# Performance work log

Hardware: AMD Instinct MI355X
Metric: run time of the kernel (lower is better)

The kernel has to match this reference:

```python
import jax, jax.numpy as jnp
import numpy as np

B, C, N = 2, 512, 2048
HEADS, DIM_HEAD, SCALE = 16, 64, 8.0
H_DIM = HEADS * DIM_HEAD
EPS = 1e-12  # F.normalize default eps


def setup_inputs() -> dict:
    key = jax.random.key(0)
    ks = jax.random.split(key, 5)
    x = jax.random.normal(ks[0], (B, C, N), dtype=jnp.float32)
    Wqkv = jax.random.normal(ks[1], (3 * H_DIM, C), dtype=jnp.float32) * (1.0 / np.sqrt(C))
    q_scale = jnp.ones((DIM_HEAD,), dtype=jnp.float32)
    k_scale = jnp.ones((DIM_HEAD,), dtype=jnp.float32)
    Wout = jax.random.normal(ks[2], (C, H_DIM), dtype=jnp.float32) * (1.0 / np.sqrt(H_DIM))
    bout = jax.random.normal(ks[3], (C,), dtype=jnp.float32) * 0.01
    return {"x": x, "Wqkv": Wqkv, "q_scale": q_scale, "k_scale": k_scale,
            "Wout": Wout, "bout": bout}


def _l2norm(t):
    # F.normalize(t, dim=-1): t / max(||t||, eps)
    n = jnp.sqrt(jnp.sum(t * t, axis=-1, keepdims=True))
    return t / jnp.maximum(n, EPS)


def reference(x, Wqkv, q_scale, k_scale, Wout, bout):
    # 1x1 conv == pointwise matmul over channel dim
    qkv = jnp.einsum('oc,bcn->bon', Wqkv, x)              # [B, 3*H_DIM, N]
    q, k, v = jnp.split(qkv, 3, axis=1)
    # unflatten channels -> [B, H, D, N]
    def to_heads(t):
        return t.reshape(B, HEADS, DIM_HEAD, N)
    q, k, v = map(to_heads, (q, k, v))
    # cosine attention: l2-normalize q,k over head dim, apply learned per-dim scales
    q = _l2norm(q.transpose(0, 1, 3, 2)) * q_scale        # [B, H, N, D]
    k = _l2norm(k.transpose(0, 1, 3, 2)) * k_scale        # [B, H, N, D]
    sim = jnp.einsum('bhid,bhjd->bhij', q, k) * SCALE     # [B, H, N, N]
    attn = jax.nn.softmax(sim, axis=-1)
    out = jnp.einsum('bhij,bhdj->bhid', attn, v)          # [B, H, N, D]
    out = out.transpose(0, 1, 3, 2).reshape(B, H_DIM, N)  # b h n d -> b (h d) n
    return jnp.einsum('oc,bcn->bon', Wout, out) + bout[None, :, None]
```

## Files before the change

kernel.cpp:

```cpp
#include <hip/hip_runtime.h>
#include <hip/hip_bf16.h>

#define BATCH 2
#define CCH   512
#define NSEQ  2048
#define HEADS 16
#define DHEAD 64
#define HDIM  1024
#define ODIM  3072
#define QK_PRESCALE 11.541560327111707f

typedef short short4v __attribute__((ext_vector_type(4)));
typedef short short8 __attribute__((ext_vector_type(8)));
typedef float float4v __attribute__((ext_vector_type(4)));
typedef int   int4v   __attribute__((ext_vector_type(4)));

__device__ __forceinline__ unsigned short f2bf(float f) {
    unsigned int u = __float_as_uint(f);
    return (unsigned short)((u + 0x7FFFu + ((u >> 16) & 1u)) >> 16);
}
__device__ __forceinline__ unsigned short f2bf_fast(float f) {
    return (unsigned short)((__float_as_uint(f) + 0x8000u) >> 16);
}
__device__ __forceinline__ float fexp2(float x) {
#if __has_builtin(__builtin_amdgcn_exp2f)
    return __builtin_amdgcn_exp2f(x);
#else
    return exp2f(x);
#endif
}
__device__ __forceinline__ int pack_bf16(float lo, float hi) {
#if __has_builtin(__builtin_amdgcn_cvt_pk_bf16_f32)
    typedef __bf16 bf2_t __attribute__((ext_vector_type(2)));
    bf2_t v = __builtin_amdgcn_cvt_pk_bf16_f32(lo, hi);
    return __builtin_bit_cast(int, v);
#else
    return (int)f2bf_fast(lo) | ((int)(unsigned)f2bf_fast(hi) << 16);
#endif
}

typedef __attribute__((address_space(1))) const void* as1_cvp;
typedef __attribute__((address_space(3))) void* as3_vp;
__device__ __forceinline__ void cp16(const void* g, void* l) {
    __builtin_amdgcn_global_load_lds((as1_cvp)g, (as3_vp)l, 16, 0, 0);
}
__global__ __launch_bounds__(256) void k_prep(
    const float* __restrict__ Wqkv, const float* __restrict__ Wout,
    const float* __restrict__ x,
    const float* __restrict__ qs, const float* __restrict__ ks,
    unsigned short* __restrict__ Wqkvb, unsigned short* __restrict__ Woutb,
    unsigned short* __restrict__ xt, float* __restrict__ M) {
    const int bx = blockIdx.x;
    if (bx < 2048) {
        if (bx == 0 && threadIdx.x < 64) {
            int lane = threadIdx.x;
            float p = fabsf(qs[lane] * ks[lane]);
#pragma unroll
            for (int off = 1; off < 64; off <<= 1) p = fmaxf(p, __shfl_xor(p, off));
            if (lane == 0) *M = QK_PRESCALE * p;
        }
        int i4 = (bx * 256 + threadIdx.x) * 4;
        const float* src; unsigned short* dst; int idx;
        if (i4 < ODIM * CCH) { src = Wqkv; dst = Wqkvb; idx = i4; }
        else { src = Wout; dst = Woutb; idx = i4 - ODIM * CCH; }
        float4 v = *(const float4*)(src + idx);
        ushort4 o;
        o.x = f2bf(v.x); o.y = f2bf(v.y); o.z = f2bf(v.z); o.w = f2bf(v.w);
        *(ushort4*)(dst + idx) = o;
        return;
    }
    __shared__ unsigned short t[64][65];
    const int fx = bx - 2048;
    const int n0 = (fx & 31) * 64;
    const int c0 = ((fx >> 5) & 7) * 64;
    const int b  = fx >> 8;
    const int tr = threadIdx.x >> 6, tc = threadIdx.x & 63;
    const float* xs = x + (size_t)b * CCH * NSEQ;
    unsigned short* xd = xt + (size_t)b * NSEQ * CCH;
#pragma unroll
    for (int r = 0; r < 16; ++r) {
        int c = r * 4 + tr;
        t[c][tc] = f2bf(xs[(size_t)(c0 + c) * NSEQ + n0 + tc]);
    }
    __syncthreads();
#pragma unroll
    for (int r = 0; r < 16; ++r) {
        int n = r * 4 + tr;
        xd[(size_t)(n0 + n) * CCH + c0 + tc] = t[tc][n];
    }
}

__global__ __launch_bounds__(256) void k_gemm_qkv(
    const unsigned short* __restrict__ W, const unsigned short* __restrict__ xt,
    const float* __restrict__ qs, const float* __restrict__ ks,
    unsigned short* __restrict__ qh, unsigned short* __restrict__ kh,
    unsigned short* __restrict__ vb) {
    constexpr int K = CCH, N = NSEQ;
    __shared__ __align__(16) short smem[2 * 128 * 64];
    short* lsA = smem;
    short* lsB = smem + 128 * 64;
    const int tid = threadIdx.x, wave = tid >> 6, lane = tid & 63;
    const int l15 = lane & 15, quad = lane >> 4;
    const int n0 = blockIdx.x * 128, m0 = blockIdx.y * 128, z = blockIdx.z;
    const short* Ab = (const short*)W + (size_t)m0 * K;
    const short* Bb = (const short*)xt + ((size_t)z * N + n0) * K;
    const int wm = wave >> 1, wn = wave & 1;
    const int cswz = (((tid & 7) ^ ((tid >> 3) & 7))) * 8;
    const int sw7 = (l15 & 7);

    float4v acc[4][4];
#pragma unroll
    for (int i = 0; i < 4; ++i)
#pragma unroll
        for (int j = 0; j < 4; ++j) acc[i][j] = (float4v){0.f, 0.f, 0.f, 0.f};

    for (int k0 = 0; k0 < K; k0 += 64) {
#pragma unroll
        for (int it = 0; it < 4; ++it) {
            int row = it * 32 + (tid >> 3);
            cp16(Ab + (size_t)row * K + k0 + cswz, &lsA[it * 2048 + wave * 512]);
            cp16(Bb + (size_t)row * K + k0 + cswz, &lsB[it * 2048 + wave * 512]);
        }
        __syncthreads();
        short8 af[4][2], bfr[4][2];
#pragma unroll
        for (int t = 0; t < 4; ++t)
#pragma unroll
            for (int kk = 0; kk < 2; ++kk) {
                af[t][kk]  = *(const short8*)&lsA[(wm * 64 + t * 16 + l15) * 64 + ((kk * 4 + quad) ^ sw7) * 8];
                bfr[t][kk] = *(const short8*)&lsB[(wn * 64 + t * 16 + l15) * 64 + ((kk * 4 + quad) ^ sw7) * 8];
            }
#pragma unroll
        for (int mt = 0; mt < 4; ++mt)
#pragma unroll
            for (int nt = 0; nt < 4; ++nt) {
                acc[mt][nt] = __builtin_amdgcn_mfma_f32_16x16x32_bf16(af[mt][0], bfr[nt][0], acc[mt][nt], 0, 0, 0);
                acc[mt][nt] = __builtin_amdgcn_mfma_f32_16x16x32_bf16(af[mt][1], bfr[nt][1], acc[mt][nt], 0, 0, 0);
            }
        __syncthreads();
    }

    const int co   = (m0 + wm * 64) >> 6;
    const int part = co >> 4;
    const int h    = co & 15;
    const int bh   = z * HEADS + h;
    short* myT = smem + wave * 4096;

    if (part < 2) {
        float inv[4];
#pragma unroll
        for (int nt = 0; nt < 4; ++nt) {
            float ss = 0.f;
#pragma unroll
            for (int mt = 0; mt < 4; ++mt)
#pragma unroll
                for (int r = 0; r < 4; ++r) ss += acc[mt][nt][r] * acc[mt][nt][r];
            ss += __shfl_xor(ss, 16);
            ss += __shfl_xor(ss, 32);
            inv[nt] = 1.0f / fmaxf(sqrtf(ss), 1e-12f);
        }
        const float* sc = part ? ks : qs;
        const float csc = part ? 1.0f : QK_PRESCALE;
#pragma unroll
        for (int mt = 0; mt < 4; ++mt) {
            const int db = mt * 16 + quad * 4;
            float4 s4 = *(const float4*)(sc + db);
            s4.x *= csc; s4.y *= csc; s4.z *= csc; s4.w *= csc;
#pragma unroll
            for (int nt = 0; nt < 4; ++nt) {
                int nl = nt * 16 + l15;
                short4v o;
                o.x = (short)f2bf(acc[mt][nt][0] * inv[nt] * s4.x);
                o.y = (short)f2bf(acc[mt][nt][1] * inv[nt] * s4.y);
                o.z = (short)f2bf(acc[mt][nt][2] * inv[nt] * s4.z);
                o.w = (short)f2bf(acc[mt][nt][3] * inv[nt] * s4.w);
                *(short4v*)&myT[nl * 64 + (((db >> 3) ^ (nl & 7)) << 3) + (db & 7)] = o;
            }
        }
        unsigned short* dst = (part ? kh : qh) + (size_t)bh * NSEQ * DHEAD
                              + (size_t)(n0 + wn * 64) * DHEAD;
#pragma unroll
        for (int pass = 0; pass < 8; ++pass) {
            int nl = pass * 8 + (lane >> 3), c = lane & 7;
            short8 vv = *(const short8*)&myT[nl * 64 + ((c ^ (nl & 7)) << 3)];
            *(short8*)&dst[(size_t)nl * DHEAD + c * 8] = vv;
        }
    } else {
#pragma unroll
        for (int mt = 0; mt < 4; ++mt)
#pragma unroll
            for (int nt = 0; nt < 4; ++nt) {
                int nl = nt * 16 + l15;
                int swc = nl >> 3, swo = nl & 7;
#pragma unroll
                for (int r = 0; r < 4; ++r) {
                    int d = mt * 16 + quad * 4 + r;
                    myT[d * 64 + ((swc ^ (d & 7)) << 3) + swo] = (short)f2bf(acc[mt][nt][r]);
                }
            }
        unsigned short* dst = vb + (size_t)bh * DHEAD * NSEQ + n0 + wn * 64;
#pragma unroll
        for (int pass = 0; pass < 8; ++pass) {
            int d = pass * 8 + (lane >> 3), c = lane & 7;
            short8 vv = *(const short8*)&myT[d * 64 + ((c ^ (d & 7)) << 3)];
            *(short8*)&dst[(size_t)d * NSEQ + c * 8] = vv;
        }
    }
}

#define KVB 32
__global__ __launch_bounds__(512, 4) void k_attn(
    const unsigned short* __restrict__ qh, const unsigned short* __restrict__ kh,
    const unsigned short* __restrict__ vb,
    unsigned short* __restrict__ aot, const float* __restrict__ Mptr) {
    __shared__ __align__(16) short Kt[2][4][KVB * 64];
    __shared__ __align__(16) short Vt[2][4][64 * KVB];
    const int tid = threadIdx.x, wave = tid >> 6, lane = tid & 63;
    const int grp = wave >> 2, w4 = wave & 3;
    const int gtid = tid & 255;
    const int l15 = lane & 15, quad = lane >> 4, q8 = quad * 8;
    const int flat = blockIdx.x;
    const int xcd = flat & 7, idx = flat >> 3;
    const int bh = xcd * 4 + (idx >> 4);
    const int i0 = (idx & 15) * 128;
    const int b = bh >> 4, h = bh & 15;
    const float Ms = *Mptr;
    const float4v mInit = (float4v){-Ms, -Ms, -Ms, -Ms};
    const int srowK = gtid >> 3;
    const int kkey  = (srowK & 3) | (((srowK >> 3) & 1) << 2);
    const int cswzK = ((gtid & 7) ^ kkey) * 8;
    const int srowV = gtid >> 2;
    const int cswzV = ((gtid & 3) ^ ((srowV >> 1) & 3)) * 8;
    const int ksw = l15 & 7;
    const int kc0 = ((0 + quad) ^ ksw) * 8;
    const int kc1 = ((4 + quad) ^ ksw) * 8;
    const int vkr = (l15 >> 1) & 3;
    const int ar0 = (l15 >> 2) * 8 + (l15 & 3);
    const int ar1 = ar0 + 4;
    const int jbase = grp * (NSEQ / 2);

    short8 qf[2][2];
    {
        const short* qb = (const short*)qh + ((size_t)bh * NSEQ + i0 + w4 * 32) * DHEAD;
#pragma unroll
        for (int it = 0; it < 2; ++it) {
            qf[it][0] = *(const short8*)&qb[(it * 16 + l15) * DHEAD + q8];
            qf[it][1] = *(const short8*)&qb[(it * 16 + l15) * DHEAD + 32 + q8];
        }
    }

    float4v of[2][4];
#pragma unroll
    for (int it = 0; it < 2; ++it)
#pragma unroll
        for (int dt = 0; dt < 4; ++dt) of[it][dt] = (float4v){0.f, 0.f, 0.f, 0.f};
    float l_acc[2] = {0.f, 0.f};

    const short* kbase = (const short*)kh + ((size_t)bh * NSEQ + jbase) * DHEAD;
    const short* vbase = (const short*)vb + (size_t)bh * DHEAD * NSEQ + jbase;

#define STAGE(T_, B_) do {                                                       \
        cp16(kbase + (size_t)((T_) * KVB + srowK) * DHEAD + cswzK,               \
             &Kt[grp][B_][w4 * 512]);                                            \
        cp16(vbase + (size_t)srowV * NSEQ + (T_) * KVB + cswzV,                  \
             &Vt[grp][B_][w4 * 512]);                                            \
    } while (0)

#define COMPUTE(CB_) do {                                                        \
        const short* Kb = &Kt[grp][CB_][0];                                      \
        const short* Vb = &Vt[grp][CB_][0];                                      \
        __builtin_amdgcn_s_setprio(1);                                           \
        short8 av[4];                                                            \
        _Pragma("unroll")                                                        \
        for (int dt = 0; dt < 4; ++dt)                                           \
            av[dt] = *(const short8*)&Vb[(dt * 16 + l15) * KVB + ((quad ^ vkr) * 8)]; \
        int4v pw[2];                                                             \
        _Pragma("unroll")                                                        \
        for (int t2 = 0; t2 < 2; ++t2) {                                         \
            const int arow = t2 ? ar1 : ar0;                                     \
            const short* kr = &Kb[arow * 64];                                    \
            short8 kf0 = *(const short8*)&kr[kc0];                               \
            short8 kf1 = *(const short8*)&kr[kc1];                               \
            _Pragma("unroll")                                                    \
            for (int it = 0; it < 2; ++it) {                                     \
                float4v s = mInit;                                               \
                s = __builtin_amdgcn_mfma_f32_16x16x32_bf16(kf0, qf[it][0], s, 0, 0, 0); \
                s = __builtin_amdgcn_mfma_f32_16x16x32_bf16(kf1, qf[it][1], s, 0, 0, 0); \
                float p0 = fexp2(s[0]);                                          \
                float p1 = fexp2(s[1]);                                          \
                float p2 = fexp2(s[2]);                                          \
                float p3 = fexp2(s[3]);                                          \
                l_acc[it] += (p0 + p1) + (p2 + p3);                              \
                pw[it][t2 * 2 + 0] = pack_bf16(p0, p1);                          \
                pw[it][t2 * 2 + 1] = pack_bf16(p2, p3);                          \
            }                                                                    \
        }                                                                        \
        {                                                                        \
            short8 pb0 = __builtin_bit_cast(short8, pw[0]);                      \
            short8 pb1 = __builtin_bit_cast(short8, pw[1]);                      \
            _Pragma("unroll")                                                    \
            for (int dt = 0; dt < 4; ++dt) {                                     \
                of[0][dt] = __builtin_amdgcn_mfma_f32_16x16x32_bf16(av[dt], pb0, of[0][dt], 0, 0, 0); \
                of[1][dt] = __builtin_amdgcn_mfma_f32_16x16x32_bf16(av[dt], pb1, of[1][dt], 0, 0, 0); \
            }                                                                    \
        }                                                                        \
        __builtin_amdgcn_s_setprio(0);                                           \
    } while (0)

    constexpr int T = (NSEQ / 2) / KVB;
    STAGE(0, 0);
    STAGE(1, 1);
    for (int t = 0; t < T - 2; ++t) {
        STAGE(t + 2, (t + 2) & 3);
        asm volatile("s_waitcnt vmcnt(4)" ::: "memory");
        __builtin_amdgcn_s_barrier();
        __builtin_amdgcn_sched_barrier(0);
        COMPUTE(t & 3);
    }
    asm volatile("s_waitcnt vmcnt(2)" ::: "memory");
    __builtin_amdgcn_s_barrier();
    __builtin_amdgcn_sched_barrier(0);
    COMPUTE((T - 2) & 3);
    asm volatile("s_waitcnt vmcnt(0)" ::: "memory");
    __builtin_amdgcn_s_barrier();
    __builtin_amdgcn_sched_barrier(0);
    COMPUTE((T - 1) & 3);
#undef STAGE
#undef COMPUTE

    float lred[2];
#pragma unroll
    for (int it = 0; it < 2; ++it) {
        float l = l_acc[it];
        l += __shfl_xor(l, 16);
        l += __shfl_xor(l, 32);
        lred[it] = l;
    }

    __syncthreads();

    float* F = (float*)&Kt[0][0][0];
    float* L = (float*)&Vt[0][0][0];
    if (grp == 1) {
#pragma unroll
        for (int it = 0; it < 2; ++it) {
#pragma unroll
            for (int dt = 0; dt < 4; ++dt)
                *(float4v*)&F[(((w4 * 2 + it) * 4 + dt) * 64 + lane) * 4] = of[it][dt];
            L[(w4 * 2 + it) * 64 + lane] = lred[it];
        }
    }
    __syncthreads();
    if (grp == 0) {
#pragma unroll
        for (int it = 0; it < 2; ++it) {
            float lt = lred[it] + L[(w4 * 2 + it) * 64 + lane];
            float inv = 1.0f / fmaxf(lt, 1e-30f);
            unsigned short* ob = aot + ((size_t)b * NSEQ + i0 + w4 * 32 + it * 16 + l15) * HDIM + h * DHEAD;
#pragma unroll
            for (int dt = 0; dt < 4; ++dt) {
                float4v p = *(const float4v*)&F[(((w4 * 2 + it) * 4 + dt) * 64 + lane) * 4];
                ushort4 o;
                o.x = f2bf((of[it][dt][0] + p[0]) * inv);
                o.y = f2bf((of[it][dt][1] + p[1]) * inv);
                o.z = f2bf((of[it][dt][2] + p[2]) * inv);
                o.w = f2bf((of[it][dt][3] + p[3]) * inv);
                *(ushort4*)&ob[dt * 16 + quad * 4] = o;
            }
        }
    }
}

__global__ __launch_bounds__(256) void k_gemm_out(
    const unsigned short* __restrict__ W, const unsigned short* __restrict__ aot,
    const float* __restrict__ bias, float* __restrict__ out) {
    constexpr int K = HDIM, N = NSEQ, M = CCH;
    __shared__ __align__(16) short lsA[64 * 64];
    __shared__ __align__(16) short lsB[64 * 64];
    const int tid = threadIdx.x, wave = tid >> 6, lane = tid & 63;
    const int l15 = lane & 15, quad = lane >> 4;
    const int n0 = blockIdx.x * 64, m0 = blockIdx.y * 64, z = blockIdx.z;
    const short* Ab = (const short*)W + (size_t)m0 * K;
    const short* Bb = (const short*)aot + ((size_t)z * N + n0) * K;
    const int wm = wave >> 1, wn = wave & 1;
    const int cswz = (((tid & 7) ^ ((tid >> 3) & 7))) * 8;
    const int sw7 = (l15 & 7);

    float4v acc[2][2];
#pragma unroll
    for (int i = 0; i < 2; ++i)
#pragma unroll
        for (int j = 0; j < 2; ++j) acc[i][j] = (float4v){0.f, 0.f, 0.f, 0.f};

    for (int k0 = 0; k0 < K; k0 += 64) {
        {
            int row = tid >> 3;
            cp16(Ab + (size_t)row * K + k0 + cswz, &lsA[wave * 512]);
            cp16(Ab + (size_t)(row + 32) * K + k0 + cswz, &lsA[2048 + wave * 512]);
            cp16(Bb + (size_t)row * K + k0 + cswz, &lsB[wave * 512]);
            cp16(Bb + (size_t)(row + 32) * K + k0 + cswz, &lsB[2048 + wave * 512]);
        }
        __syncthreads();
        short8 af[2][2], bfr[2][2];
#pragma unroll
        for (int t = 0; t < 2; ++t)
#pragma unroll
            for (int kk = 0; kk < 2; ++kk) {
                af[t][kk]  = *(const short8*)&lsA[(wm * 32 + t * 16 + l15) * 64 + ((kk * 4 + quad) ^ sw7) * 8];
                bfr[t][kk] = *(const short8*)&lsB[(wn * 32 + t * 16 + l15) * 64 + ((kk * 4 + quad) ^ sw7) * 8];
            }
#pragma unroll
        for (int mt = 0; mt < 2; ++mt)
#pragma unroll
            for (int nt = 0; nt < 2; ++nt) {
                acc[mt][nt] = __builtin_amdgcn_mfma_f32_16x16x32_bf16(af[mt][0], bfr[nt][0], acc[mt][nt], 0, 0, 0);
                acc[mt][nt] = __builtin_amdgcn_mfma_f32_16x16x32_bf16(af[mt][1], bfr[nt][1], acc[mt][nt], 0, 0, 0);
            }
        __syncthreads();
    }
    float* Co = out + (size_t)z * M * N;
#pragma unroll
    for (int mt = 0; mt < 2; ++mt)
#pragma unroll
        for (int nt = 0; nt < 2; ++nt) {
            int mrow = m0 + wm * 32 + mt * 16 + quad * 4;
#pragma unroll
            for (int r = 0; r < 4; ++r) {
                int mr = mrow + r;
                int nc = n0 + wn * 32 + nt * 16 + l15;
                Co[(size_t)mr * N + nc] = acc[mt][nt][r] + bias[mr];
            }
        }
}

extern "C" void kernel_launch(void* const* d_in, const int* in_sizes, int n_in,
                              void* d_out, int out_size, void* d_ws, size_t ws_size,
                              hipStream_t stream) {
    const float* x = nullptr; const float* Wqkv = nullptr;
    const float* qs = nullptr; const float* ks = nullptr;
    const float* Wout = nullptr; const float* bout = nullptr;
    for (int i = 0; i < n_in; ++i) {
        switch (in_sizes[i]) {
            case BATCH * CCH * NSEQ: x    = (const float*)d_in[i]; break;
            case ODIM * CCH:         Wqkv = (const float*)d_in[i]; break;
            case CCH * HDIM:         Wout = (const float*)d_in[i]; break;
            case CCH:                bout = (const float*)d_in[i]; break;
            case DHEAD: if (!qs) qs = (const float*)d_in[i]; else ks = (const float*)d_in[i]; break;
            default: break;
        }
    }
    float* y = (float*)d_out;

    char* ws = (char*)d_ws;
    float*          Mbuf  = (float*)(ws + 0);
    unsigned short* Wqkvb = (unsigned short*)(ws + 4096);
    unsigned short* Woutb = (unsigned short*)(ws + 3149824);
    unsigned short* xt    = (unsigned short*)(ws + 4198400);
    unsigned short* qh    = (unsigned short*)(ws + 8392704);
    unsigned short* kh    = (unsigned short*)(ws + 16781312);
    unsigned short* vb    = (unsigned short*)(ws + 25169920);
    unsigned short* aot   = (unsigned short*)(ws + 33558528);

    k_prep<<<dim3(2048 + 512), 256, 0, stream>>>(Wqkv, Wout, x, qs, ks, Wqkvb, Woutb, xt, Mbuf);
    k_gemm_qkv<<<dim3(NSEQ / 128, ODIM / 128, BATCH), 256, 0, stream>>>(Wqkvb, xt, qs, ks, qh, kh, vb);
    k_attn<<<dim3(512), 512, 0, stream>>>(qh, kh, vb, aot, Mbuf);
    k_gemm_out<<<dim3(NSEQ / 64, CCH / 64, BATCH), 256, 0, stream>>>(Woutb, aot, bout, y);
}
```

Before: 149.1 us.

## Software-pipeline P·V MFMAs of the previous tile behind current QK and exp

Restructures the attention inner loop so the P·V MFMAs for the previous KV tile are issued right after the current tile's QK^T MFMAs, before the exp2 and pack work. The four QK MFMA chains are interleaved, and the V fragments and packed probabilities are carried in registers across iterations. This is meant to overlap MFMA work with the VALU exponentials and break the serial QK→exp→PV dependency within a step. A prologue, an epilogue PV flush and unroll-by-4 of the main loop are added, which raises register pressure.

After: 142.9 us. 4.2% less time.

```diff
diff --git a/kernel.cpp b/kernel.cpp
--- a/kernel.cpp
+++ b/kernel.cpp
@@ -259,6 +259,8 @@
     const short* kbase = (const short*)kh + ((size_t)bh * NSEQ + jbase) * DHEAD;
     const short* vbase = (const short*)vb + (size_t)bh * DHEAD * NSEQ + jbase;
 
+    short8 pb0c, pb1c, avc[4];
+
 #define STAGE(T_, B_) do {                                                       \
         cp16(kbase + (size_t)((T_) * KVB + srowK) * DHEAD + cswzK,               \
              &Kt[grp][B_][w4 * 512]);                                            \
@@ -266,67 +268,83 @@
              &Vt[grp][B_][w4 * 512]);                                            \
     } while (0)
 
-#define COMPUTE(CB_) do {                                                        \
+#define STEP(CB_, DO_PV_) do {                                                   \
         const short* Kb = &Kt[grp][CB_][0];                                      \
         const short* Vb = &Vt[grp][CB_][0];                                      \
         __builtin_amdgcn_s_setprio(1);                                           \
-        short8 av[4];                                                            \
+        short8 k00 = *(const short8*)&Kb[ar0 * 64 + kc0];                        \
+        short8 k01 = *(const short8*)&Kb[ar0 * 64 + kc1];                        \
+        short8 k10 = *(const short8*)&Kb[ar1 * 64 + kc0];                        \
+        short8 k11 = *(const short8*)&Kb[ar1 * 64 + kc1];                        \
+        float4v s00 = __builtin_amdgcn_mfma_f32_16x16x32_bf16(k00, qf[0][0], mInit, 0, 0, 0); \
+        float4v s01 = __builtin_amdgcn_mfma_f32_16x16x32_bf16(k00, qf[1][0], mInit, 0, 0, 0); \
+        float4v s10 = __builtin_amdgcn_mfma_f32_16x16x32_bf16(k10, qf[0][0], mInit, 0, 0, 0); \
+        float4v s11 = __builtin_amdgcn_mfma_f32_16x16x32_bf16(k10, qf[1][0], mInit, 0, 0, 0); \
+        s00 = __builtin_amdgcn_mfma_f32_16x16x32_bf16(k01, qf[0][1], s00, 0, 0, 0); \
+        s01 = __builtin_amdgcn_mfma_f32_16x16x32_bf16(k01, qf[1][1], s01, 0, 0, 0); \
+        s10 = __builtin_amdgcn_mfma_f32_16x16x32_bf16(k11, qf[0][1], s10, 0, 0, 0); \
+        s11 = __builtin_amdgcn_mfma_f32_16x16x32_bf16(k11, qf[1][1], s11, 0, 0, 0); \
+        if (DO_PV_) {                                                            \
+            _Pragma("unroll")                                                    \
+            for (int dt = 0; dt < 4; ++dt) {                                     \
+                of[0][dt] = __builtin_amdgcn_mfma_f32_16x16x32_bf16(avc[dt], pb0c, of[0][dt], 0, 0, 0); \
+                of[1][dt] = __builtin_amdgcn_mfma_f32_16x16x32_bf16(avc[dt], pb1c, of[1][dt], 0, 0, 0); \
+            }                                                                    \
+        }                                                                        \
+        int4v pw0, pw1;                                                          \
+        {                                                                        \
+            float p0, p1, p2, p3;                                                \
+            p0 = fexp2(s00[0]); p1 = fexp2(s00[1]); p2 = fexp2(s00[2]); p3 = fexp2(s00[3]); \
+            l_acc[0] += (p0 + p1) + (p2 + p3);                                   \
+            pw0[0] = pack_bf16(p0, p1); pw0[1] = pack_bf16(p2, p3);              \
+            p0 = fexp2(s10[0]); p1 = fexp2(s10[1]); p2 = fexp2(s10[2]); p3 = fexp2(s10[3]); \
+            l_acc[0] += (p0 + p1) + (p2 + p3);                                   \
+            pw0[2] = pack_bf16(p0, p1); pw0[3] = pack_bf16(p2, p3);              \
+            p0 = fexp2(s01[0]); p1 = fexp2(s01[1]); p2 = fexp2(s01[2]); p3 = fexp2(s01[3]); \
+            l_acc[1] += (p0 + p1) + (p2 + p3);                                   \
+            pw1[0] = pack_bf16(p0, p1); pw1[1] = pack_bf16(p2, p3);              \
+            p0 = fexp2(s11[0]); p1 = fexp2(s11[1]); p2 = fexp2(s11[2]); p3 = fexp2(s11[3]); \
+            l_acc[1] += (p0 + p1) + (p2 + p3);                                   \
+            pw1[2] = pack_bf16(p0, p1); pw1[3] = pack_bf16(p2, p3);              \
+        }                                                                        \
+        pb0c = __builtin_bit_cast(short8, pw0);                                  \
+        pb1c = __builtin_bit_cast(short8, pw1);                                  \
         _Pragma("unroll")                                                        \
         for (int dt = 0; dt < 4; ++dt)                                           \
-            av[dt] = *(const short8*)&Vb[(dt * 16 + l15) * KVB + ((quad ^ vkr) * 8)]; \
-        int4v pw[2];                                                             \
-        _Pragma("unroll")                                                        \
-        for (int t2 = 0; t2 < 2; ++t2) {                                         \
-            const int arow = t2 ? ar1 : ar0;                                     \
-            const short* kr = &Kb[arow * 64];                                    \
-            short8 kf0 = *(const short8*)&kr[kc0];                               \
-            short8 kf1 = *(const short8*)&kr[kc1];                               \
-            _Pragma("unroll")                                                    \
-            for (int it = 0; it < 2; ++it) {                                     \
-                float4v s = mInit;                                               \
-                s = __builtin_amdgcn_mfma_f32_16x16x32_bf16(kf0, qf[it][0], s, 0, 0, 0); \
-                s = __builtin_amdgcn_mfma_f32_16x16x32_bf16(kf1, qf[it][1], s, 0, 0, 0); \
-                float p0 = fexp2(s[0]);                                          \
-                float p1 = fexp2(s[1]);                                          \
-                float p2 = fexp2(s[2]);                                          \
-                float p3 = fexp2(s[3]);                                          \
-                l_acc[it] += (p0 + p1) + (p2 + p3);                              \
-                pw[it][t2 * 2 + 0] = pack_bf16(p0, p1);                          \
-                pw[it][t2 * 2 + 1] = pack_bf16(p2, p3);                          \
-            }                                                                    \
-        }                                                                        \
-        {                                                                        \
-            short8 pb0 = __builtin_bit_cast(short8, pw[0]);                      \
-            short8 pb1 = __builtin_bit_cast(short8, pw[1]);                      \
-            _Pragma("unroll")                                                    \
-            for (int dt = 0; dt < 4; ++dt) {                                     \
-                of[0][dt] = __builtin_amdgcn_mfma_f32_16x16x32_bf16(av[dt], pb0, of[0][dt], 0, 0, 0); \
-                of[1][dt] = __builtin_amdgcn_mfma_f32_16x16x32_bf16(av[dt], pb1, of[1][dt], 0, 0, 0); \
-            }                                                                    \
-        }                                                                        \
+            avc[dt] = *(const short8*)&Vb[(dt * 16 + l15) * KVB + ((quad ^ vkr) * 8)]; \
         __builtin_amdgcn_s_setprio(0);                                           \
+    } while (0)
+
+#define WAITBAR(N_) do {                                                         \
+        asm volatile("s_waitcnt vmcnt(" #N_ ")" ::: "memory");                   \
+        __builtin_amdgcn_s_barrier();                                            \
+        __builtin_amdgcn_sched_barrier(0);                                       \
     } while (0)
 
     constexpr int T = (NSEQ / 2) / KVB;
     STAGE(0, 0);
     STAGE(1, 1);
-    for (int t = 0; t < T - 2; ++t) {
+    STAGE(2, 2);
+    WAITBAR(4);
+    STEP(0, 0);
+#pragma unroll 4
+    for (int t = 1; t <= T - 3; ++t) {
         STAGE(t + 2, (t + 2) & 3);
-        asm volatile("s_waitcnt vmcnt(4)" ::: "memory");
-        __builtin_amdgcn_s_barrier();
-        __builtin_amdgcn_sched_barrier(0);
-        COMPUTE(t & 3);
-    }
-    asm volatile("s_waitcnt vmcnt(2)" ::: "memory");
-    __builtin_amdgcn_s_barrier();
-    __builtin_amdgcn_sched_barrier(0);
-    COMPUTE((T - 2) & 3);
-    asm volatile("s_waitcnt vmcnt(0)" ::: "memory");
-    __builtin_amdgcn_s_barrier();
-    __builtin_amdgcn_sched_barrier(0);
-    COMPUTE((T - 1) & 3);
+        WAITBAR(4);
+        STEP(t & 3, 1);
+    }
+    WAITBAR(2);
+    STEP((T - 2) & 3, 1);
+    WAITBAR(0);
+    STEP((T - 1) & 3, 1);
+#pragma unroll
+    for (int dt = 0; dt < 4; ++dt) {
+        of[0][dt] = __builtin_amdgcn_mfma_f32_16x16x32_bf16(avc[dt], pb0c, of[0][dt], 0, 0, 0);
+        of[1][dt] = __builtin_amdgcn_mfma_f32_16x16x32_bf16(avc[dt], pb1c, of[1][dt], 0, 0, 0);
+    }
 #undef STAGE
-#undef COMPUTE
+#undef STEP
+#undef WAITBAR
 
     float lred[2];
 #pragma unroll
```
